# Performance work log

Hardware: AMD Instinct MI355X
Metric: run time of the kernel (lower is better)

## Reference

```python
import jax, jax.numpy as jnp
import numpy as np


def _update_cv(features, labels, ave, cov, amount, class_num):
    # Segment-reduce formulation of the onehot-expand update_CV.
    N, A = features.shape
    C = class_num
    counts = jax.ops.segment_sum(jnp.ones((N,), features.dtype), labels, num_segments=C)  # [C]
    sums = jax.ops.segment_sum(features, labels, num_segments=C)  # [C, A]
    denom = jnp.where(counts == 0, 1.0, counts)[:, None]  # Amount_CxA with zeros -> 1
    ave_CxA = sums / denom
    # var_temp: sum over samples of (x - mean_label)^2, divided by count
    diff = features - ave_CxA[labels]  # [N, A]
    sq = jax.ops.segment_sum(diff * diff, labels, num_segments=C)
    var_temp = sq / denom
    sum_weight = counts[:, None]  # [C,1] broadcast over A
    weight_CV = sum_weight / (sum_weight + amount[:, None])
    weight_CV = jnp.nan_to_num(weight_CV, nan=0.0)
    additional_CV = weight_CV * (1 - weight_CV) * (ave - ave_CxA) ** 2
    new_cov = cov * (1 - weight_CV) + var_temp * weight_CV + additional_CV
    new_ave = ave * (1 - weight_CV) + ave_CxA * weight_CV
    new_amount = amount + counts
    return new_ave, new_cov, new_amount


def _isda_aug(fc_weight, y, labels, cv_matrix, ratio):
    # sigma2[n,c] = ratio * sum_a (W[c,a] - W[labels[n],a])^2 * CV[labels[n],a]
    # = ratio * ( (W^2) @ cv_n - 2 W @ (w_n * cv_n) + sum_a w_n^2 cv_n )
    cv_n = cv_matrix[labels]              # [N, A]
    w_n = fc_weight[labels]               # [N, A]
    t1 = cv_n @ (fc_weight ** 2).T        # [N, C]
    t2 = (w_n * cv_n) @ fc_weight.T       # [N, C]
    t3 = jnp.sum(w_n * w_n * cv_n, axis=1, keepdims=True)  # [N, 1]
    sigma2 = ratio * (t1 - 2.0 * t2 + t3)
    return y + 0.5 * sigma2


def setup_inputs() -> dict:
    key = jax.random.key(0)
    k1, k2, k3, k4 = jax.random.split(key, 4)
    N, A, C = 512, 2048, 1000
    features = jax.random.normal(k1, (N, A), dtype=jnp.float32)
    labels = jax.random.randint(k2, (N,), 0, C)
    fc_weight = jax.random.normal(k3, (C, A), dtype=jnp.float32) * 0.02
    fc_bias = jax.random.normal(k4, (C,), dtype=jnp.float32) * 0.02
    return {
        "features": features,
        "labels": labels,
        "fc_weight": fc_weight,
        "fc_bias": fc_bias,
        "ave_state": jnp.zeros((C, A), jnp.float32),
        "cov_state": jnp.zeros((C, A), jnp.float32),
        "amount_state": jnp.zeros((C,), jnp.float32),
        "ratio": 1,
    }


def reference(features, labels, fc_weight, fc_bias, ave_state, cov_state, amount_state, ratio):
    C = fc_weight.shape[0]
    # model head: y = features @ W^T + b (features come from backbone; detached for CV)
    y = features @ fc_weight.T + fc_bias
    new_ave, new_cov, new_amount = _update_cv(
        jax.lax.stop_gradient(features), labels, ave_state, cov_state, amount_state, C)
    isda_y = _isda_aug(fc_weight, y, labels, jax.lax.stop_gradient(new_cov), ratio)
    log_probs = jax.nn.log_softmax(isda_y, axis=1)
    loss = -jnp.mean(jnp.take_along_axis(log_probs, labels[:, None], axis=1))
    return loss, y, new_ave, new_cov, new_amount
```

## Files before the change

### kernel.cpp

```cpp
#include <hip/hip_runtime.h>
#include <hip/hip_bf16.h>

typedef short v8s __attribute__((ext_vector_type(8)));
typedef float v4f __attribute__((ext_vector_type(4)));

#define KSPLIT 4

static __device__ __forceinline__ float ldv(const void* p, size_t i, int f32m) {
    if (f32m) return ((const float*)p)[i];
    return __bfloat162float(((const __hip_bfloat16*)p)[i]);
}
static __device__ __forceinline__ void stv(void* p, size_t i, float v, int f32m) {
    if (f32m) ((float*)p)[i] = v;
    else ((__hip_bfloat16*)p)[i] = __float2bfloat16(v);
}
static __device__ __forceinline__ unsigned short f2bu(float x) {
    __hip_bfloat16 h = __float2bfloat16(x);
    return *(unsigned short*)&h;
}
static __device__ __forceinline__ float bu2f(unsigned short u) {
    return __uint_as_float(((unsigned)u) << 16);
}

static __device__ __forceinline__ float decode_scalar(const void* p) {
    unsigned u = *(const unsigned*)p;
    unsigned e32 = (u >> 23) & 0xff;
    if (e32 >= 97 && e32 <= 160) return __uint_as_float(u);
    unsigned lo = u & 0xffffu;
    unsigned e16 = (lo >> 7) & 0xff;
    if ((u >> 16) == 0 && e16 >= 97 && e16 <= 160)
        return __uint_as_float(lo << 16);
    return (float)(int)u;
}

static __device__ __forceinline__ int block_sniff(const void* feat) {
    const __hip_bfloat16* p = (const __hip_bfloat16*)feat;
    float v = __bfloat162float(p[threadIdx.x & 255]);
    int bad = !(fabsf(v) < 1e10f);
    return __syncthreads_or(bad) ? 1 : 0;
}

__device__ __forceinline__ float wave_sum(float v) {
    #pragma unroll
    for (int o = 32; o > 0; o >>= 1) v += __shfl_down(v, o, 64);
    return v;
}
__device__ __forceinline__ float wave_max(float v) {
    #pragma unroll
    for (int o = 32; o > 0; o >>= 1) v = fmaxf(v, __shfl_down(v, o, 64));
    return v;
}

static __device__ __forceinline__ void ld16(unsigned short* lds, const unsigned short* g) {
    __builtin_amdgcn_global_load_lds(
        (const __attribute__((address_space(1))) unsigned int*)g,
        (__attribute__((address_space(3))) unsigned int*)lds,
        16, 0, 0);
}

__global__ __launch_bounds__(256) void prep_sort(
        const void* __restrict__ feat, unsigned short* __restrict__ featb, int total,
        const int* __restrict__ labels, int* __restrict__ counts,
        int* __restrict__ offs, int* __restrict__ rows,
        float* __restrict__ misc, int Nn, int C) {
    int f32m = block_sniff(feat);
    int tid = threadIdx.x;
    int i = (blockIdx.x * 256 + tid) * 8;
    if (i < total) {
        if (f32m) {
            const float* f = (const float*)feat + i;
            unsigned short r[8];
            #pragma unroll
            for (int u = 0; u < 8; ++u) r[u] = f2bu(f[u]);
            *(v8s*)(featb + i) = *(v8s*)r;
        } else {
            *(v8s*)(featb + i) = *(const v8s*)((const unsigned short*)feat + i);
        }
    }
    if (blockIdx.x != 0) return;

    if (tid < 16) misc[tid] = 0.f;

    __shared__ int h[1024];
    __shared__ int ex[256];
    __shared__ int cur[1024];
    #pragma unroll
    for (int u = 0; u < 4; ++u) h[tid + 256 * u] = 0;
    __syncthreads();
    for (int k = tid; k < Nn; k += 256) atomicAdd(&h[labels[k]], 1);
    __syncthreads();
    int b0 = h[4 * tid], b1 = h[4 * tid + 1], b2 = h[4 * tid + 2], b3 = h[4 * tid + 3];
    int s = b0 + b1 + b2 + b3;
    ex[tid] = s;
    __syncthreads();
    for (int d = 1; d < 256; d <<= 1) {
        int v = (tid >= d) ? ex[tid - d] : 0;
        __syncthreads();
        ex[tid] += v;
        __syncthreads();
    }
    int excl = ex[tid] - s;
    int o0 = excl, o1 = o0 + b0, o2 = o1 + b1, o3 = o2 + b2;
    counts[4 * tid] = b0; counts[4 * tid + 1] = b1;
    counts[4 * tid + 2] = b2; counts[4 * tid + 3] = b3;
    offs[4 * tid] = o0; offs[4 * tid + 1] = o1;
    offs[4 * tid + 2] = o2; offs[4 * tid + 3] = o3;
    cur[4 * tid] = o0; cur[4 * tid + 1] = o1;
    cur[4 * tid + 2] = o2; cur[4 * tid + 3] = o3;
    __syncthreads();
    for (int k = tid; k < Nn; k += 256) {
        int pos = atomicAdd(&cur[labels[k]], 1);
        rows[pos] = k;
    }
}

__global__ __launch_bounds__(256) void finalize_stats(
        const unsigned short* __restrict__ featb,
        const int* __restrict__ counts, const int* __restrict__ offs,
        const int* __restrict__ rows,
        const void* __restrict__ ave, const void* __restrict__ cov,
        const void* __restrict__ amount, const void* __restrict__ W,
        const void* __restrict__ feat,
        void* __restrict__ out, size_t off_ave, size_t off_cov, size_t off_amt,
        unsigned short* __restrict__ Wb, unsigned short* __restrict__ W2b,
        unsigned short* __restrict__ Cb, unsigned short* __restrict__ Gb,
        float* __restrict__ T3p, int A, int A8) {
    __shared__ float sb[4];
    int f32m = block_sniff(feat);
    int c = blockIdx.y;
    int a = blockIdx.x * 256 + threadIdx.x;
    size_t idx = (size_t)c * A + a;
    int cnti = counts[c];
    int start = offs[c];
    float s1 = 0.f, s2 = 0.f;
    for (int i = 0; i < cnti; ++i) {
        float x = bu2f(featb[(size_t)rows[start + i] * A + a]);
        s1 += x;
        s2 += x * x;
    }
    float cnt = (float)cnti;
    float denom = cnti > 0 ? cnt : 1.f;
    float mean = s1 / denom;
    float var = fmaxf((s2 - cnt * mean * mean) / denom, 0.f);
    float amt = ldv(amount, c, f32m);
    float tot = cnt + amt;
    float w = tot > 0.f ? (cnt / tot) : 0.f;
    float av = ldv(ave, idx, f32m);
    float cv = ldv(cov, idx, f32m);
    float d = av - mean;
    float ncv = cv * (1.f - w) + var * w + w * (1.f - w) * d * d;
    float nav = av * (1.f - w) + mean * w;
    stv(out, off_cov + idx, ncv, f32m);
    stv(out, off_ave + idx, nav, f32m);
    float wv = ldv(W, idx, f32m);
    Wb[idx] = f2bu(wv);
    W2b[idx] = f2bu(wv * wv);
    Cb[idx] = f2bu(ncv);
    Gb[idx] = f2bu(ncv * wv);
    if (a == 0) stv(out, off_amt + c, amt + cnt, f32m);
    float s = wave_sum(wv * wv * ncv);
    int lane = threadIdx.x & 63, wid = threadIdx.x >> 6;
    if (lane == 0) sb[wid] = s;
    __syncthreads();
    if (threadIdx.x == 0) T3p[(size_t)c * A8 + blockIdx.x] = sb[0] + sb[1] + sb[2] + sb[3];
}

__global__ __launch_bounds__(256) void triple_gemm_mfma(
        const unsigned short* __restrict__ featb,
        const unsigned short* __restrict__ Wb,
        const unsigned short* __restrict__ W2b,
        const unsigned short* __restrict__ Cb,
        const unsigned short* __restrict__ Gb,
        const int* __restrict__ labels,
        float* __restrict__ partY, float* __restrict__ partT1, float* __restrict__ partT2,
        int Cpad, int A, size_t NC) {
    __shared__ unsigned short sA[20480];
    __shared__ int sLab[64];
    int tid = threadIdx.x, wv = tid >> 6, lane = tid & 63;
    int n0 = blockIdx.y * 64, j0 = blockIdx.x * 64;
    int kslice = A / KSPLIT;
    int k0 = blockIdx.z * kslice;
    if (tid < 64) sLab[tid] = labels[n0 + tid];
    __syncthreads();

    int r = lane & 15, q = lane >> 4;
    int fr = wv * 16 + r;
    const unsigned short* pF = featb + (size_t)(n0 + fr) * A + k0 + q * 8;
    int lab = sLab[fr];
    const unsigned short* pC = Cb + (size_t)lab * A + k0 + q * 8;
    const unsigned short* pG = Gb + (size_t)lab * A + k0 + q * 8;
    const unsigned short* pW = Wb  + (size_t)(j0 + fr) * A + k0 + q * 8;
    const unsigned short* pQ = W2b + (size_t)(j0 + fr) * A + k0 + q * 8;
    unsigned short* dF = &sA[0     + wv * 1024];
    unsigned short* dC = &sA[4096  + wv * 1024];
    unsigned short* dG = &sA[8192  + wv * 1024];
    unsigned short* dW = &sA[12288 + wv * 1024];
    unsigned short* dQ = &sA[16384 + wv * 1024];

    v4f aY[4] = {{0,0,0,0},{0,0,0,0},{0,0,0,0},{0,0,0,0}};
    v4f aT1[4] = {{0,0,0,0},{0,0,0,0},{0,0,0,0},{0,0,0,0}};
    v4f aT2[4] = {{0,0,0,0},{0,0,0,0},{0,0,0,0},{0,0,0,0}};

    for (int kk = 0; kk < kslice; kk += 64) {
        ld16(dF, pF); ld16(dF + 512, pF + 32);
        ld16(dC, pC); ld16(dC + 512, pC + 32);
        ld16(dG, pG); ld16(dG + 512, pG + 32);
        ld16(dW, pW); ld16(dW + 512, pW + 32);
        ld16(dQ, pQ); ld16(dQ + 512, pQ + 32);
        pF += 64; pC += 64; pG += 64; pW += 64; pQ += 64;
        __syncthreads();
        #pragma unroll
        for (int s = 0; s < 2; ++s) {
            v8s f = *(v8s*)&sA[0    + wv * 1024 + s * 512 + lane * 8];
            v8s c = *(v8s*)&sA[4096 + wv * 1024 + s * 512 + lane * 8];
            v8s g = *(v8s*)&sA[8192 + wv * 1024 + s * 512 + lane * 8];
            #pragma unroll
            for (int t = 0; t < 4; ++t) {
                v8s w  = *(v8s*)&sA[12288 + t * 1024 + s * 512 + lane * 8];
                v8s w2 = *(v8s*)&sA[16384 + t * 1024 + s * 512 + lane * 8];
                aY[t]  = __builtin_amdgcn_mfma_f32_16x16x32_bf16(f, w,  aY[t],  0, 0, 0);
                aT1[t] = __builtin_amdgcn_mfma_f32_16x16x32_bf16(c, w2, aT1[t], 0, 0, 0);
                aT2[t] = __builtin_amdgcn_mfma_f32_16x16x32_bf16(g, w,  aT2[t], 0, 0, 0);
            }
        }
        __syncthreads();
    }

    float* pY = partY + (size_t)blockIdx.z * NC;
    float* p1 = partT1 + (size_t)blockIdx.z * NC;
    float* p2 = partT2 + (size_t)blockIdx.z * NC;
    int quad = lane >> 4, colb = lane & 15;
    #pragma unroll
    for (int t = 0; t < 4; ++t) {
        int j = j0 + t * 16 + colb;
        #pragma unroll
        for (int rr = 0; rr < 4; ++rr) {
            int n = n0 + wv * 16 + quad * 4 + rr;
            size_t idx = (size_t)n * Cpad + j;
            pY[idx] = aY[t][rr];
            p1[idx] = aT1[t][rr];
            p2[idx] = aT2[t][rr];
        }
    }
}

__global__ __launch_bounds__(256) void epilogue_rowloss(
        const float* __restrict__ partY, const float* __restrict__ partT1,
        const float* __restrict__ partT2, const float* __restrict__ T3p,
        const void* __restrict__ bias, const void* __restrict__ feat,
        const int* __restrict__ labels,
        void* __restrict__ out, size_t off_y,
        float* __restrict__ misc,
        int C, int Cpad, int A8, const void* ratio_p, size_t NC, int Nn) {
    __shared__ float sb[4];
    __shared__ float sM;
    __shared__ float sLabVal;
    int f32m = block_sniff(feat);
    int tid = threadIdx.x;
    int n = blockIdx.x;
    int lab = labels[n];
    float t3 = 0.f;
    for (int i = 0; i < A8; ++i) t3 += T3p[(size_t)lab * A8 + i];
    float ratio = decode_scalar(ratio_p);

    float vals[8];
    int nu = Cpad >> 8;
    float m = -3.4e38f;
    for (int u = 0; u < nu; ++u) {
        int j = u * 256 + tid;
        float v = -3.4e38f;
        if (j < C) {
            size_t idx = (size_t)n * Cpad + j;
            float y = 0.f, t1 = 0.f, t2 = 0.f;
            #pragma unroll
            for (int z = 0; z < KSPLIT; ++z) {
                y  += partY[z * NC + idx];
                t1 += partT1[z * NC + idx];
                t2 += partT2[z * NC + idx];
            }
            y += ldv(bias, j, f32m);
            stv(out, off_y + (size_t)n * C + j, y, f32m);
            v = y + 0.5f * ratio * (t1 - 2.f * t2 + t3);
            if (j == lab) sLabVal = v;
        }
        vals[u] = v;
        m = fmaxf(m, v);
    }
    m = wave_max(m);
    int lane = tid & 63, wid = tid >> 6;
    if (lane == 0) sb[wid] = m;
    __syncthreads();
    if (tid == 0) sM = fmaxf(fmaxf(sb[0], sb[1]), fmaxf(sb[2], sb[3]));
    __syncthreads();
    m = sM;
    float s = 0.f;
    for (int u = 0; u < nu; ++u) s += expf(vals[u] - m);
    __syncthreads();
    s = wave_sum(s);
    if (lane == 0) sb[wid] = s;
    __syncthreads();
    if (tid == 0) {
        float rl = m + logf(sb[0] + sb[1] + sb[2] + sb[3]) - sLabVal;
        atomicAdd(&misc[0], rl);
        __threadfence();
        int old = atomicAdd((int*)&misc[1], 1);
        if (old == Nn - 1) {
            __threadfence();
            float tot = atomicAdd(&misc[0], 0.f);
            stv(out, 0, tot / (float)Nn, f32m);
        }
    }
}

extern "C" void kernel_launch(void* const* d_in, const int* in_sizes, int n_in,
                              void* d_out, int out_size, void* d_ws, size_t ws_size,
                              hipStream_t stream) {
    const void* feat   = d_in[0];
    const int*  labels = (const int*)d_in[1];
    const void* W      = d_in[2];
    const void* bias   = d_in[3];
    const void* ave    = d_in[4];
    const void* cov    = d_in[5];
    const void* amount = d_in[6];
    const void* ratiop = d_in[7];

    int NA = in_sizes[0];
    int Nn = in_sizes[1];
    int C  = in_sizes[3];
    int A  = NA / Nn;
    int CA = in_sizes[2];
    int Cpad = ((C + 255) / 256) * 256;
    int A8 = A / 256;
    size_t NC = (size_t)Nn * Cpad;

    size_t off_y   = 1;
    size_t off_ave = off_y + (size_t)Nn * C;
    size_t off_cov = off_ave + (size_t)CA;
    size_t off_amt = off_cov + (size_t)CA;

    char* ws = (char*)d_ws;
    int*   w_cnt  = (int*)ws;
    int*   w_off  = w_cnt + 1024;
    int*   w_rows = w_off + 1024;
    float* w_misc = (float*)(w_rows + 1024);
    float* w_T3p  = w_misc + 16;
    float* w_partY  = w_T3p + 8192;
    float* w_partT1 = w_partY + KSPLIT * NC;
    float* w_partT2 = w_partT1 + KSPLIT * NC;
    unsigned short* w_featb = (unsigned short*)(w_partT2 + KSPLIT * NC);
    unsigned short* w_Wb    = w_featb + NA;
    unsigned short* w_W2b   = w_Wb + CA;
    unsigned short* w_Cb    = w_W2b + CA;
    unsigned short* w_Gb    = w_Cb + CA;

    prep_sort<<<NA / 2048, 256, 0, stream>>>(feat, w_featb, NA, labels,
                                             w_cnt, w_off, w_rows, w_misc, Nn, C);
    dim3 g2(A8, C);
    finalize_stats<<<g2, 256, 0, stream>>>(w_featb, w_cnt, w_off, w_rows,
                                           ave, cov, amount, W, feat,
                                           d_out, off_ave, off_cov, off_amt,
                                           w_Wb, w_W2b, w_Cb, w_Gb, w_T3p, A, A8);
    dim3 g3(Cpad / 64, Nn / 64, KSPLIT);
    triple_gemm_mfma<<<g3, 256, 0, stream>>>(w_featb, w_Wb, w_W2b, w_Cb, w_Gb,
                                             labels, w_partY, w_partT1, w_partT2,
                                             Cpad, A, NC);
    epilogue_rowloss<<<Nn, 256, 0, stream>>>(w_partY, w_partT1, w_partT2, w_T3p,
                                             bias, feat, labels, d_out, off_y,
                                             w_misc, C, Cpad, A8, ratiop, NC, Nn);
}
```

Before: 146.7 us.

## Vectorize stats and epilogue loads, halve GEMM K-step LDS tile

```diff
diff --git a/kernel.cpp b/kernel.cpp
--- a/kernel.cpp
+++ b/kernel.cpp
@@ -3,6 +3,7 @@
 
 typedef short v8s __attribute__((ext_vector_type(8)));
 typedef float v4f __attribute__((ext_vector_type(4)));
+typedef unsigned short u16;
 
 #define KSPLIT 4
 
@@ -14,12 +15,18 @@
     if (f32m) ((float*)p)[i] = v;
     else ((__hip_bfloat16*)p)[i] = __float2bfloat16(v);
 }
-static __device__ __forceinline__ unsigned short f2bu(float x) {
+static __device__ __forceinline__ u16 f2bu(float x) {
     __hip_bfloat16 h = __float2bfloat16(x);
-    return *(unsigned short*)&h;
-}
-static __device__ __forceinline__ float bu2f(unsigned short u) {
+    return *(u16*)&h;
+}
+static __device__ __forceinline__ float bu2f(u16 u) {
     return __uint_as_float(((unsigned)u) << 16);
+}
+static __device__ __forceinline__ v4f ldv4(const void* p, size_t i, int f32m) {
+    if (f32m) return *(const v4f*)((const float*)p + i);
+    ushort4 u = *(const ushort4*)((const u16*)p + i);
+    v4f r; r[0] = bu2f(u.x); r[1] = bu2f(u.y); r[2] = bu2f(u.z); r[3] = bu2f(u.w);
+    return r;
 }
 
 static __device__ __forceinline__ float decode_scalar(const void* p) {
@@ -51,7 +58,7 @@
     return v;
 }
 
-static __device__ __forceinline__ void ld16(unsigned short* lds, const unsigned short* g) {
+static __device__ __forceinline__ void ld16(u16* lds, const u16* g) {
     __builtin_amdgcn_global_load_lds(
         (const __attribute__((address_space(1))) unsigned int*)g,
         (__attribute__((address_space(3))) unsigned int*)lds,
@@ -59,7 +66,7 @@
 }
 
 __global__ __launch_bounds__(256) void prep_sort(
-        const void* __restrict__ feat, unsigned short* __restrict__ featb, int total,
+        const void* __restrict__ feat, u16* __restrict__ featb, int total,
         const int* __restrict__ labels, int* __restrict__ counts,
         int* __restrict__ offs, int* __restrict__ rows,
         float* __restrict__ misc, int Nn, int C) {
@@ -69,12 +76,12 @@
     if (i < total) {
         if (f32m) {
             const float* f = (const float*)feat + i;
-            unsigned short r[8];
+            u16 r[8];
             #pragma unroll
             for (int u = 0; u < 8; ++u) r[u] = f2bu(f[u]);
             *(v8s*)(featb + i) = *(v8s*)r;
         } else {
-            *(v8s*)(featb + i) = *(const v8s*)((const unsigned short*)feat + i);
+            *(v8s*)(featb + i) = *(const v8s*)((const u16*)feat + i);
         }
     }
     if (blockIdx.x != 0) return;
@@ -115,66 +122,80 @@
 }
 
 __global__ __launch_bounds__(256) void finalize_stats(
-        const unsigned short* __restrict__ featb,
+        const u16* __restrict__ featb,
         const int* __restrict__ counts, const int* __restrict__ offs,
         const int* __restrict__ rows,
         const void* __restrict__ ave, const void* __restrict__ cov,
         const void* __restrict__ amount, const void* __restrict__ W,
         const void* __restrict__ feat,
         void* __restrict__ out, size_t off_ave, size_t off_cov, size_t off_amt,
-        unsigned short* __restrict__ Wb, unsigned short* __restrict__ W2b,
-        unsigned short* __restrict__ Cb, unsigned short* __restrict__ Gb,
-        float* __restrict__ T3p, int A, int A8) {
+        u16* __restrict__ Wb, u16* __restrict__ W2b,
+        u16* __restrict__ Cb, u16* __restrict__ Gb,
+        float* __restrict__ T3p, int A, int nch) {
     __shared__ float sb[4];
     int f32m = block_sniff(feat);
+    int tid = threadIdx.x;
     int c = blockIdx.y;
-    int a = blockIdx.x * 256 + threadIdx.x;
-    size_t idx = (size_t)c * A + a;
+    int a0 = blockIdx.x * 1024 + tid * 4;
+    size_t idx = (size_t)c * A + a0;
     int cnti = counts[c];
     int start = offs[c];
-    float s1 = 0.f, s2 = 0.f;
+    v4f s1 = {0,0,0,0}, s2 = {0,0,0,0};
     for (int i = 0; i < cnti; ++i) {
-        float x = bu2f(featb[(size_t)rows[start + i] * A + a]);
-        s1 += x;
-        s2 += x * x;
+        ushort4 xu = *(const ushort4*)(featb + (size_t)rows[start + i] * A + a0);
+        float x0 = bu2f(xu.x), x1 = bu2f(xu.y), x2 = bu2f(xu.z), x3 = bu2f(xu.w);
+        s1[0] += x0; s1[1] += x1; s1[2] += x2; s1[3] += x3;
+        s2[0] += x0 * x0; s2[1] += x1 * x1; s2[2] += x2 * x2; s2[3] += x3 * x3;
     }
     float cnt = (float)cnti;
     float denom = cnti > 0 ? cnt : 1.f;
-    float mean = s1 / denom;
-    float var = fmaxf((s2 - cnt * mean * mean) / denom, 0.f);
     float amt = ldv(amount, c, f32m);
     float tot = cnt + amt;
     float w = tot > 0.f ? (cnt / tot) : 0.f;
-    float av = ldv(ave, idx, f32m);
-    float cv = ldv(cov, idx, f32m);
-    float d = av - mean;
-    float ncv = cv * (1.f - w) + var * w + w * (1.f - w) * d * d;
-    float nav = av * (1.f - w) + mean * w;
-    stv(out, off_cov + idx, ncv, f32m);
-    stv(out, off_ave + idx, nav, f32m);
-    float wv = ldv(W, idx, f32m);
-    Wb[idx] = f2bu(wv);
-    W2b[idx] = f2bu(wv * wv);
-    Cb[idx] = f2bu(ncv);
-    Gb[idx] = f2bu(ncv * wv);
-    if (a == 0) stv(out, off_amt + c, amt + cnt, f32m);
-    float s = wave_sum(wv * wv * ncv);
-    int lane = threadIdx.x & 63, wid = threadIdx.x >> 6;
+    v4f av = ldv4(ave, idx, f32m);
+    v4f cv = ldv4(cov, idx, f32m);
+    v4f wv = ldv4(W, idx, f32m);
+    ushort4 oW, oW2, oC, oG;
+    u16* pW = (u16*)&oW; u16* pW2 = (u16*)&oW2; u16* pC = (u16*)&oC; u16* pG = (u16*)&oG;
+    float t3a = 0.f;
+    #pragma unroll
+    for (int e = 0; e < 4; ++e) {
+        float mean = s1[e] / denom;
+        float var = fmaxf((s2[e] - cnt * mean * mean) / denom, 0.f);
+        float d = av[e] - mean;
+        float ncv = cv[e] * (1.f - w) + var * w + w * (1.f - w) * d * d;
+        float nav = av[e] * (1.f - w) + mean * w;
+        stv(out, off_cov + idx + e, ncv, f32m);
+        stv(out, off_ave + idx + e, nav, f32m);
+        float wq = wv[e];
+        pW[e] = f2bu(wq);
+        pW2[e] = f2bu(wq * wq);
+        pC[e] = f2bu(ncv);
+        pG[e] = f2bu(ncv * wq);
+        t3a += wq * wq * ncv;
+    }
+    *(ushort4*)(Wb + idx) = oW;
+    *(ushort4*)(W2b + idx) = oW2;
+    *(ushort4*)(Cb + idx) = oC;
+    *(ushort4*)(Gb + idx) = oG;
+    if (a0 == 0) stv(out, off_amt + c, amt + cnt, f32m);
+    float s = wave_sum(t3a);
+    int lane = tid & 63, wid = tid >> 6;
     if (lane == 0) sb[wid] = s;
     __syncthreads();
-    if (threadIdx.x == 0) T3p[(size_t)c * A8 + blockIdx.x] = sb[0] + sb[1] + sb[2] + sb[3];
+    if (tid == 0) T3p[(size_t)c * nch + blockIdx.x] = sb[0] + sb[1] + sb[2] + sb[3];
 }
 
 __global__ __launch_bounds__(256) void triple_gemm_mfma(
-        const unsigned short* __restrict__ featb,
-        const unsigned short* __restrict__ Wb,
-        const unsigned short* __restrict__ W2b,
-        const unsigned short* __restrict__ Cb,
-        const unsigned short* __restrict__ Gb,
+        const u16* __restrict__ featb,
+        const u16* __restrict__ Wb,
+        const u16* __restrict__ W2b,
+        const u16* __restrict__ Cb,
+        const u16* __restrict__ Gb,
         const int* __restrict__ labels,
         float* __restrict__ partY, float* __restrict__ partT1, float* __restrict__ partT2,
         int Cpad, int A, size_t NC) {
-    __shared__ unsigned short sA[20480];
+    __shared__ u16 sA[10240];
     __shared__ int sLab[64];
     int tid = threadIdx.x, wv = tid >> 6, lane = tid & 63;
     int n0 = blockIdx.y * 64, j0 = blockIdx.x * 64;
@@ -185,43 +206,36 @@
 
     int r = lane & 15, q = lane >> 4;
     int fr = wv * 16 + r;
-    const unsigned short* pF = featb + (size_t)(n0 + fr) * A + k0 + q * 8;
+    const u16* pF = featb + (size_t)(n0 + fr) * A + k0 + q * 8;
     int lab = sLab[fr];
-    const unsigned short* pC = Cb + (size_t)lab * A + k0 + q * 8;
-    const unsigned short* pG = Gb + (size_t)lab * A + k0 + q * 8;
-    const unsigned short* pW = Wb  + (size_t)(j0 + fr) * A + k0 + q * 8;
-    const unsigned short* pQ = W2b + (size_t)(j0 + fr) * A + k0 + q * 8;
-    unsigned short* dF = &sA[0     + wv * 1024];
-    unsigned short* dC = &sA[4096  + wv * 1024];
-    unsigned short* dG = &sA[8192  + wv * 1024];
-    unsigned short* dW = &sA[12288 + wv * 1024];
-    unsigned short* dQ = &sA[16384 + wv * 1024];
+    const u16* pC = Cb + (size_t)lab * A + k0 + q * 8;
+    const u16* pG = Gb + (size_t)lab * A + k0 + q * 8;
+    const u16* pW = Wb  + (size_t)(j0 + fr) * A + k0 + q * 8;
+    const u16* pQ = W2b + (size_t)(j0 + fr) * A + k0 + q * 8;
+    u16* dF = &sA[0    + wv * 512];
+    u16* dC = &sA[2048 + wv * 512];
+    u16* dG = &sA[4096 + wv * 512];
+    u16* dW = &sA[6144 + wv * 512];
+    u16* dQ = &sA[8192 + wv * 512];
 
     v4f aY[4] = {{0,0,0,0},{0,0,0,0},{0,0,0,0},{0,0,0,0}};
     v4f aT1[4] = {{0,0,0,0},{0,0,0,0},{0,0,0,0},{0,0,0,0}};
     v4f aT2[4] = {{0,0,0,0},{0,0,0,0},{0,0,0,0},{0,0,0,0}};
 
-    for (int kk = 0; kk < kslice; kk += 64) {
-        ld16(dF, pF); ld16(dF + 512, pF + 32);
-        ld16(dC, pC); ld16(dC + 512, pC + 32);
-        ld16(dG, pG); ld16(dG + 512, pG + 32);
-        ld16(dW, pW); ld16(dW + 512, pW + 32);
-        ld16(dQ, pQ); ld16(dQ + 512, pQ + 32);
-        pF += 64; pC += 64; pG += 64; pW += 64; pQ += 64;
+    for (int kk = 0; kk < kslice; kk += 32) {
+        ld16(dF, pF); ld16(dC, pC); ld16(dG, pG); ld16(dW, pW); ld16(dQ, pQ);
+        pF += 32; pC += 32; pG += 32; pW += 32; pQ += 32;
         __syncthreads();
+        v8s f = *(v8s*)&sA[0    + wv * 512 + lane * 8];
+        v8s c = *(v8s*)&sA[2048 + wv * 512 + lane * 8];
+        v8s g = *(v8s*)&sA[4096 + wv * 512 + lane * 8];
         #pragma unroll
-        for (int s = 0; s < 2; ++s) {
-            v8s f = *(v8s*)&sA[0    + wv * 1024 + s * 512 + lane * 8];
-            v8s c = *(v8s*)&sA[4096 + wv * 1024 + s * 512 + lane * 8];
-            v8s g = *(v8s*)&sA[8192 + wv * 1024 + s * 512 + lane * 8];
-            #pragma unroll
-            for (int t = 0; t < 4; ++t) {
-                v8s w  = *(v8s*)&sA[12288 + t * 1024 + s * 512 + lane * 8];
-                v8s w2 = *(v8s*)&sA[16384 + t * 1024 + s * 512 + lane * 8];
-                aY[t]  = __builtin_amdgcn_mfma_f32_16x16x32_bf16(f, w,  aY[t],  0, 0, 0);
-                aT1[t] = __builtin_amdgcn_mfma_f32_16x16x32_bf16(c, w2, aT1[t], 0, 0, 0);
-                aT2[t] = __builtin_amdgcn_mfma_f32_16x16x32_bf16(g, w,  aT2[t], 0, 0, 0);
-            }
+        for (int t = 0; t < 4; ++t) {
+            v8s w  = *(v8s*)&sA[6144 + t * 512 + lane * 8];
+            v8s w2 = *(v8s*)&sA[8192 + t * 512 + lane * 8];
+            aY[t]  = __builtin_amdgcn_mfma_f32_16x16x32_bf16(f, w,  aY[t],  0, 0, 0);
+            aT1[t] = __builtin_amdgcn_mfma_f32_16x16x32_bf16(c, w2, aT1[t], 0, 0, 0);
+            aT2[t] = __builtin_amdgcn_mfma_f32_16x16x32_bf16(g, w,  aT2[t], 0, 0, 0);
         }
         __syncthreads();
     }
@@ -251,7 +265,7 @@
         const int* __restrict__ labels,
         void* __restrict__ out, size_t off_y,
         float* __restrict__ misc,
-        int C, int Cpad, int A8, const void* ratio_p, size_t NC, int Nn) {
+        int C, int Cpad, int nch, const void* ratio_p, size_t NC, int Nn) {
     __shared__ float sb[4];
     __shared__ float sM;
     __shared__ float sLabVal;
@@ -260,30 +274,31 @@
     int n = blockIdx.x;
     int lab = labels[n];
     float t3 = 0.f;
-    for (int i = 0; i < A8; ++i) t3 += T3p[(size_t)lab * A8 + i];
+    for (int i = 0; i < nch; ++i) t3 += T3p[(size_t)lab * nch + i];
     float ratio = decode_scalar(ratio_p);
 
-    float vals[8];
-    int nu = Cpad >> 8;
+    int j0 = tid * 4;
+    size_t idx = (size_t)n * Cpad + j0;
+    v4f y = {0,0,0,0}, t1 = {0,0,0,0}, t2 = {0,0,0,0};
+    #pragma unroll
+    for (int z = 0; z < KSPLIT; ++z) {
+        y  += *(const v4f*)(partY  + z * NC + idx);
+        t1 += *(const v4f*)(partT1 + z * NC + idx);
+        t2 += *(const v4f*)(partT2 + z * NC + idx);
+    }
+    v4f vals;
     float m = -3.4e38f;
-    for (int u = 0; u < nu; ++u) {
-        int j = u * 256 + tid;
+    #pragma unroll
+    for (int e = 0; e < 4; ++e) {
+        int j = j0 + e;
         float v = -3.4e38f;
         if (j < C) {
-            size_t idx = (size_t)n * Cpad + j;
-            float y = 0.f, t1 = 0.f, t2 = 0.f;
-            #pragma unroll
-            for (int z = 0; z < KSPLIT; ++z) {
-                y  += partY[z * NC + idx];
-                t1 += partT1[z * NC + idx];
-                t2 += partT2[z * NC + idx];
-            }
-            y += ldv(bias, j, f32m);
-            stv(out, off_y + (size_t)n * C + j, y, f32m);
-            v = y + 0.5f * ratio * (t1 - 2.f * t2 + t3);
+            float yv = y[e] + ldv(bias, j, f32m);
+            stv(out, off_y + (size_t)n * C + j, yv, f32m);
+            v = yv + 0.5f * ratio * (t1[e] - 2.f * t2[e] + t3);
             if (j == lab) sLabVal = v;
         }
-        vals[u] = v;
+        vals[e] = v;
         m = fmaxf(m, v);
     }
     m = wave_max(m);
@@ -294,7 +309,8 @@
     __syncthreads();
     m = sM;
     float s = 0.f;
-    for (int u = 0; u < nu; ++u) s += expf(vals[u] - m);
+    #pragma unroll
+    for (int e = 0; e < 4; ++e) s += expf(vals[e] - m);
     __syncthreads();
     s = wave_sum(s);
     if (lane == 0) sb[wid] = s;
@@ -330,7 +346,7 @@
     int A  = NA / Nn;
     int CA = in_sizes[2];
     int Cpad = ((C + 255) / 256) * 256;
-    int A8 = A / 256;
+    int nch = A / 1024;
     size_t NC = (size_t)Nn * Cpad;
 
     size_t off_y   = 1;
@@ -347,24 +363,24 @@
     float* w_partY  = w_T3p + 8192;
     float* w_partT1 = w_partY + KSPLIT * NC;
     float* w_partT2 = w_partT1 + KSPLIT * NC;
-    unsigned short* w_featb = (unsigned short*)(w_partT2 + KSPLIT * NC);
-    unsigned short* w_Wb    = w_featb + NA;
-    unsigned short* w_W2b   = w_Wb + CA;
-    unsigned short* w_Cb    = w_W2b + CA;
-    unsigned short* w_Gb    = w_Cb + CA;
+    u16* w_featb = (u16*)(w_partT2 + KSPLIT * NC);
+    u16* w_Wb    = w_featb + NA;
+    u16* w_W2b   = w_Wb + CA;
+    u16* w_Cb    = w_W2b + CA;
+    u16* w_Gb    = w_Cb + CA;
 
     prep_sort<<<NA / 2048, 256, 0, stream>>>(feat, w_featb, NA, labels,
                                              w_cnt, w_off, w_rows, w_misc, Nn, C);
-    dim3 g2(A8, C);
+    dim3 g2(nch, C);
     finalize_stats<<<g2, 256, 0, stream>>>(w_featb, w_cnt, w_off, w_rows,
                                            ave, cov, amount, W, feat,
                                            d_out, off_ave, off_cov, off_amt,
-                                           w_Wb, w_W2b, w_Cb, w_Gb, w_T3p, A, A8);
+                                           w_Wb, w_W2b, w_Cb, w_Gb, w_T3p, A, nch);
     dim3 g3(Cpad / 64, Nn / 64, KSPLIT);
     triple_gemm_mfma<<<g3, 256, 0, stream>>>(w_featb, w_Wb, w_W2b, w_Cb, w_Gb,
                                              labels, w_partY, w_partT1, w_partT2,
                                              Cpad, A, NC);
     epilogue_rowloss<<<Nn, 256, 0, stream>>>(w_partY, w_partT1, w_partT2, w_T3p,
                                              bias, feat, labels, d_out, off_y,
-                                             w_misc, C, Cpad, A8, ratiop, NC, Nn);
-}
+                                             w_misc, C, Cpad, nch, ratiop, NC, Nn);
+}
```

Result: no change. 148.8 us (+1.5%).
